# Performance work log

Measured on AMD Instinct MI355X. Metric: run time of the kernel, lower is better.

## Reference

```python
import jax, jax.numpy as jnp
import numpy as np

N_TRANSFORMS = 24
N_INIT = 5
SOFT_BLEND = 5.0
MAX_STEPS = 8   # reduced from 50 for reference runtime; same per-step math
CVG = 1e-5
DVG = 1.0
EPS = 1e-6


def posi_enc(x):
    # min_deg=0, max_deg=4, append_identity: [...,3] -> [...,27]
    scales = jnp.asarray([1.0, 2.0, 4.0, 8.0], x.dtype)
    xb = (x[..., None, :] * scales[:, None]).reshape(x.shape[:-1] + (12,))
    return jnp.concatenate([x, jnp.sin(xb), jnp.cos(xb)], axis=-1)


def mlp(h, params):
    for W, b in params[:-1]:
        h = jax.nn.relu(h @ W + b)
    W, b = params[-1]
    return h @ W + b


def setup_inputs() -> dict:
    key = jax.random.key(0)
    ks = jax.random.split(key, 16)
    B, N, J = 1, 32768, N_TRANSFORMS
    x = jax.random.normal(ks[0], (B, N, 3), jnp.float32)
    bone_pts = jax.random.normal(ks[1], (J, 3), jnp.float32)

    def near_id(k):
        A = jnp.eye(4, dtype=jnp.float32) + 0.05 * jax.random.normal(k, (J, 4, 4), jnp.float32)
        return A.at[:, 3, :].set(jnp.asarray([0.0, 0.0, 0.0, 1.0], jnp.float32))

    inp = dict(
        x=x, bone_pts=bone_pts,
        transforms=near_id(ks[2]), delta_transforms=near_id(ks[3]),
        W0=0.1 * jax.random.normal(ks[4], (27, 128), jnp.float32), b0=jnp.zeros((128,), jnp.float32),
        W1=0.1 * jax.random.normal(ks[5], (128, 128), jnp.float32), b1=jnp.zeros((128,), jnp.float32),
        W2=0.1 * jax.random.normal(ks[6], (128, 128), jnp.float32), b2=jnp.zeros((128,), jnp.float32),
        W3=0.1 * jax.random.normal(ks[7], (128, 128), jnp.float32), b3=jnp.zeros((128,), jnp.float32),
        W4=0.1 * jax.random.normal(ks[8], (128, 25), jnp.float32), b4=jnp.zeros((25,), jnp.float32),
    )
    return inp


def reference(x, bone_pts, transforms, delta_transforms, W0, b0, W1, b1, W2, b2, W3, b3, W4, b4):
    params = [(W0, b0), (W1, b1), (W2, b2), (W3, b3), (W4, b4)]
    B, N, _ = x.shape
    I = N_INIT + 1  # with_bkgd appends identity init
    dt = x.dtype

    # ---- _initialize_canonical: KNN over bone distances, gather delta transforms
    d = jnp.linalg.norm(x[:, :, None, :] - bone_pts, axis=-1)          # [B,N,J]
    idx = jax.lax.top_k(-d, N_INIT)[1]                                  # [B,N,5]
    Tsel = delta_transforms[idx]                                        # [B,N,5,4,4]
    eye4 = jnp.broadcast_to(jnp.eye(4, dtype=dt), (B, N, 1, 4, 4))
    Tinit = jnp.concatenate([Tsel, eye4], axis=2)                       # [B,N,I,4,4]
    xh = jnp.concatenate([x, jnp.ones_like(x[..., :1])], axis=-1)
    xc0 = jnp.einsum('bnipq,bnq->bnip', Tinit[..., :3, :4], xh)         # [B,N,I,3]

    M = B * N * I
    target = jnp.broadcast_to(x[:, :, None, :], (B, N, I, 3)).reshape(M, 3)
    x0 = xc0.reshape(M, 3)
    Tfull = jnp.concatenate([transforms, jnp.eye(4, dtype=dt)[None]], axis=0)  # [J+1,4,4]

    def g(xc):  # forward-skinning residual g(x_cano) = LBS(x_cano) - x_world
        w = jax.nn.softmax(SOFT_BLEND * mlp(posi_enc(xc), params), axis=-1)   # [M,25]
        tf = jnp.einsum('mj,jpq->mpq', w, Tfull)                               # [M,4,4]
        return jnp.einsum('mpq,mq->mp', tf[:, :3, :3], xc) + tf[:, :3, 3] - target

    # ---- Broyden with dense per-point masking (replaces torch boolean indexing)
    Jinv0 = jnp.broadcast_to(jnp.eye(3, dtype=dt), (M, 3, 3))
    gx0 = g(x0)
    upd0 = -(Jinv0 @ gx0[:, :, None])[:, :, 0]
    norm0 = jnp.linalg.norm(gx0, axis=-1)
    zeros3 = jnp.zeros((M, 3), dt)
    state = (x0, gx0, Jinv0, upd0, x0, norm0, zeros3, zeros3, jnp.ones((M,), bool))

    def body(_, s):
        xk, gx, Jinv, upd, xopt, nopt, dx, dgx, mask = s
        m3 = mask[:, None]
        dx = jnp.where(m3, upd, dx)
        xk = jnp.where(m3, xk + dx, xk)
        gnew = g(xk)
        dgx = jnp.where(m3, gnew - gx, dgx)
        gx = jnp.where(m3, gx + dgx, gx)
        gn = jnp.linalg.norm(gx, axis=-1)
        better = gn < nopt
        nopt = jnp.where(better, gn, nopt)
        xopt = jnp.where(better[:, None], xk, xopt)
        mask = (nopt > CVG) & (gn < DVG)
        vT = dx[:, None, :] @ Jinv                                      # [M,1,3]
        a = dx[:, :, None] - Jinv @ dgx[:, :, None]                      # [M,3,1]
        b = vT @ dgx[:, :, None]                                         # [M,1,1]
        b = b + jnp.where(b >= 0, EPS, -EPS)
        Jinv = jnp.where(mask[:, None, None], Jinv + (a / b) @ vT, Jinv)
        upd = jnp.where(m3, -(Jinv @ gx[:, :, None])[:, :, 0], upd)
        return (xk, gx, Jinv, upd, xopt, nopt, dx, dgx, mask)

    state = jax.lax.fori_loop(0, MAX_STEPS, body, state)
    xopt, nopt = state[4], state[5]
    xopt = jax.lax.stop_gradient(xopt)  # torch detaches the root solve
    valid = nopt < CVG

    # differentiable final forward skinning at the found canonical points
    w = jax.nn.softmax(SOFT_BLEND * mlp(posi_enc(xopt), params), axis=-1)
    tf = jnp.einsum('mj,jpq->mpq', w, Tfull)
    xw = jnp.einsum('mpq,mq->mp', tf[:, :3, :3], xopt) + tf[:, :3, 3]

    return (xw.reshape(B, N, I, 3), xopt.reshape(B, N, I, 3),
            nopt.reshape(B, N, I), valid.reshape(B, N, I))
```

## Files before the change

kernel.cpp:

```cpp
#include <hip/hip_runtime.h>
#include <math.h>

#define BLOCK 256
#define PPB 64
#define HP 132
#define WCOLS 2136

typedef float v2f __attribute__((ext_vector_type(2)));

__device__ __forceinline__ v2f mkv2(float a, float b) {
    v2f r; r.x = a; r.y = b; return r;
}
__device__ __forceinline__ v2f pkfma(v2f a, v2f b, v2f c) {
#if __has_builtin(__builtin_elementwise_fma)
    return __builtin_elementwise_fma(a, b, c);
#else
    return mkv2(fmaf(a.x, b.x, c.x), fmaf(a.y, b.y, c.y));
#endif
}
__device__ __forceinline__ float f4el(const float4& v, int r) {
    return (r == 0) ? v.x : (r == 1) ? v.y : (r == 2) ? v.z : v.w;
}
__device__ __forceinline__ int col_base(int p) { return p * HP + ((p >> 2) << 3); }

__global__ void prep_kernel(const float* __restrict__ W0, const float* __restrict__ W4,
                            const float* __restrict__ b4, float* __restrict__ W0p,
                            float* __restrict__ W4p, float* __restrict__ b4p) {
    const int t = blockIdx.x * blockDim.x + threadIdx.x;
    if (t < 32 * 128) {
        const int k = t >> 7, j = t & 127;
        W0p[t] = (k < 27) ? W0[k * 128 + j] : 0.0f;
    }
    if (t < 128 * 32) {
        const int k = t >> 5, j = t & 31;
        W4p[t] = (j < 25) ? W4[k * 25 + j] : 0.0f;
    }
    if (t < 32) b4p[t] = (t < 25) ? b4[t] : 0.0f;
}

template <int K, int WS>
__device__ __forceinline__ void layerM(const float* __restrict__ Wc,
                                       const float* __restrict__ bc,
                                       const float* hg, float* hwr) {
    constexpr int NB = K / 4;
    v2f acc[16];
    {
        const float4 b0 = *(const float4*)(bc);
        const float4 b1 = *(const float4*)(bc + 4);
#pragma unroll
        for (int p = 0; p < 4; ++p) {
            acc[p * 4 + 0] = mkv2(b0.x, b0.y);
            acc[p * 4 + 1] = mkv2(b0.z, b0.w);
            acc[p * 4 + 2] = mkv2(b1.x, b1.y);
            acc[p * 4 + 3] = mkv2(b1.z, b1.w);
        }
    }
#pragma unroll 2
    for (int kb = 0; kb < NB; ++kb) {
        float4 h4[4];
#pragma unroll
        for (int p = 0; p < 4; ++p)
            h4[p] = *(const float4*)(hg + p * HP + kb * 4);
        float4 w0[4], w1[4];
#pragma unroll
        for (int r = 0; r < 4; ++r) {
            w0[r] = *(const float4*)(Wc + (kb * 4 + r) * WS);
            w1[r] = *(const float4*)(Wc + (kb * 4 + r) * WS + 4);
        }
#pragma unroll
        for (int r = 0; r < 4; ++r) {
            const v2f wa = mkv2(w0[r].x, w0[r].y);
            const v2f wb = mkv2(w0[r].z, w0[r].w);
            const v2f wc = mkv2(w1[r].x, w1[r].y);
            const v2f wd = mkv2(w1[r].z, w1[r].w);
#pragma unroll
            for (int p = 0; p < 4; ++p) {
                const float hv = f4el(h4[p], r);
                const v2f hh = mkv2(hv, hv);
                acc[p * 4 + 0] = pkfma(hh, wa, acc[p * 4 + 0]);
                acc[p * 4 + 1] = pkfma(hh, wb, acc[p * 4 + 1]);
                acc[p * 4 + 2] = pkfma(hh, wc, acc[p * 4 + 2]);
                acc[p * 4 + 3] = pkfma(hh, wd, acc[p * 4 + 3]);
            }
        }
    }
#pragma unroll
    for (int p = 0; p < 4; ++p) {
        float4 o0, o1;
        o0.x = fmaxf(acc[p * 4 + 0].x, 0.f); o0.y = fmaxf(acc[p * 4 + 0].y, 0.f);
        o0.z = fmaxf(acc[p * 4 + 1].x, 0.f); o0.w = fmaxf(acc[p * 4 + 1].y, 0.f);
        o1.x = fmaxf(acc[p * 4 + 2].x, 0.f); o1.y = fmaxf(acc[p * 4 + 2].y, 0.f);
        o1.z = fmaxf(acc[p * 4 + 3].x, 0.f); o1.w = fmaxf(acc[p * 4 + 3].y, 0.f);
        *(float4*)(hwr + p * HP) = o0;
        *(float4*)(hwr + p * HP + 4) = o1;
    }
}

__global__ __launch_bounds__(BLOCK)
__attribute__((amdgpu_num_vgpr(128))) void snarf_kernel(
    const float* __restrict__ xin, const float* __restrict__ bone_pts,
    const float* __restrict__ transforms, const float* __restrict__ delta_tf,
    const float* __restrict__ W0p, const float* __restrict__ b0,
    const float* __restrict__ W1, const float* __restrict__ b1,
    const float* __restrict__ W2, const float* __restrict__ b2,
    const float* __restrict__ W3, const float* __restrict__ b3,
    const float* __restrict__ W4p, const float* __restrict__ b4p,
    float* __restrict__ out, int Npts) {
    __shared__ float hL[4 * WCOLS];
    __shared__ float stL[25 * PPB];
    const int tid = threadIdx.x;
    const int wid = tid >> 6;
    const int lane = tid & 63;
    const int p16 = lane & 15;
    const int sq = lane >> 4;
    const int cg = lane >> 2;
    const int gg = lane & 3;
    const int M = Npts * 6;
    const int m = blockIdx.x * PPB + wid * 16 + p16;
    const int mc = (m < M) ? m : (M - 1);
    const int n = mc / 6;
    const int i = mc - n * 6;

    float* hWv = &hL[wid * WCOLS];
    const float* hg = hWv + gg * 536;
    float* hwr = hWv + gg * 536 + 8 * cg;
    float* hq = hWv + col_base(p16);
    volatile float* st = &stL[wid * 16 + p16];
#define STS(idx) st[(idx) * PPB]

    const float tx = xin[n * 3 + 0], ty = xin[n * 3 + 1], tz = xin[n * 3 + 2];

    float xk0, xk1, xk2;
    if (i < 5) {
        float dprev = -1.0f;
        int jprev = -1;
        for (int r = 0; r <= i; ++r) {
            float bd = 3.4028235e38f;
            int bj = 0;
            for (int j = 0; j < 24; ++j) {
                const float ax = tx - bone_pts[j * 3 + 0];
                const float ay = ty - bone_pts[j * 3 + 1];
                const float az = tz - bone_pts[j * 3 + 2];
                const float d = sqrtf(ax * ax + ay * ay + az * az);
                const bool taken = (d < dprev) || (d == dprev && j <= jprev);
                if (!taken && d < bd) { bd = d; bj = j; }
            }
            dprev = bd;
            jprev = bj;
        }
        const float* T = delta_tf + jprev * 16;
        xk0 = fmaf(T[0], tx, fmaf(T[1], ty, fmaf(T[2], tz, T[3])));
        xk1 = fmaf(T[4], tx, fmaf(T[5], ty, fmaf(T[6], tz, T[7])));
        xk2 = fmaf(T[8], tx, fmaf(T[9], ty, fmaf(T[10], tz, T[11])));
    } else {
        xk0 = tx; xk1 = ty; xk2 = tz;
    }

    float gx0 = 0.f, gx1 = 0.f, gx2 = 0.f;
    bool mask = (m < M);

    for (int step = -1; step < 8; ++step) {
        bool m3 = mask;
        if (step >= 0) {
            if (__ballot(mask) == 0ull) break;
            if (m3) {
                const float u0 = STS(9), u1 = STS(10), u2 = STS(11);
                STS(12) = u0; STS(13) = u1; STS(14) = u2;
                xk0 += u0; xk1 += u1; xk2 += u2;
            }
        }
        const float cx0 = xk0, cx1 = xk1, cx2 = xk2;

        {
            const float f = (float)(1 << sq);
            float sx, cxv, sy, cyv, sz, czv;
            sincosf(f * cx0, &sx, &cxv);
            sincosf(f * cx1, &sy, &cyv);
            sincosf(f * cx2, &sz, &czv);
            if (sq == 0) { hq[0] = cx0; hq[1] = cx1; hq[2] = cx2; }
            const int sb = 3 + sq * 3;
            hq[sb + 0] = sx;  hq[sb + 1] = sy;  hq[sb + 2] = sz;
            hq[sb + 12] = cxv; hq[sb + 13] = cyv; hq[sb + 14] = czv;
            if (sq == 3) {
                hq[27] = 0.f; hq[28] = 0.f; hq[29] = 0.f; hq[30] = 0.f; hq[31] = 0.f;
            }
        }

        __builtin_amdgcn_s_setprio(1);
        layerM<32, 128>(W0p + 8 * cg, b0 + 8 * cg, hg, hwr);
        layerM<128, 128>(W1 + 8 * cg, b1 + 8 * cg, hg, hwr);
        layerM<128, 128>(W2 + 8 * cg, b2 + 8 * cg, hg, hwr);
        layerM<128, 128>(W3 + 8 * cg, b3 + 8 * cg, hg, hwr);

        {
            v2f la[4];
            const float* bc = b4p + 8 * sq;
            const float4 bb0 = *(const float4*)(bc);
            const float4 bb1 = *(const float4*)(bc + 4);
            la[0] = mkv2(bb0.x, bb0.y); la[1] = mkv2(bb0.z, bb0.w);
            la[2] = mkv2(bb1.x, bb1.y); la[3] = mkv2(bb1.z, bb1.w);
            const float* Wc = W4p + 8 * sq;
#pragma unroll 2
            for (int kb = 0; kb < 32; ++kb) {
                const float4 h4 = *(const float4*)(hq + kb * 4);
#pragma unroll
                for (int r = 0; r < 4; ++r) {
                    const int k = kb * 4 + r;
                    const float4 w0 = *(const float4*)(Wc + k * 32);
                    const float4 w1 = *(const float4*)(Wc + k * 32 + 4);
                    const float hv = f4el(h4, r);
                    const v2f hh = mkv2(hv, hv);
                    la[0] = pkfma(hh, mkv2(w0.x, w0.y), la[0]);
                    la[1] = pkfma(hh, mkv2(w0.z, w0.w), la[1]);
                    la[2] = pkfma(hh, mkv2(w1.x, w1.y), la[2]);
                    la[3] = pkfma(hh, mkv2(w1.z, w1.w), la[3]);
                }
            }
            __builtin_amdgcn_s_setprio(0);
            float4 o0, o1;
            o0.x = la[0].x; o0.y = la[0].y; o0.z = la[1].x; o0.w = la[1].y;
            o1.x = la[2].x; o1.y = la[2].y; o1.z = la[3].x; o1.w = la[3].y;
            *(float4*)(hq + 8 * sq) = o0;
            *(float4*)(hq + 8 * sq + 4) = o1;
        }

        float l25[25];
        {
            const float4 r0 = *(const float4*)(hq + 0);
            const float4 r1 = *(const float4*)(hq + 4);
            const float4 r2 = *(const float4*)(hq + 8);
            const float4 r3 = *(const float4*)(hq + 12);
            const float4 r4 = *(const float4*)(hq + 16);
            const float4 r5 = *(const float4*)(hq + 20);
            l25[0] = r0.x; l25[1] = r0.y; l25[2] = r0.z; l25[3] = r0.w;
            l25[4] = r1.x; l25[5] = r1.y; l25[6] = r1.z; l25[7] = r1.w;
            l25[8] = r2.x; l25[9] = r2.y; l25[10] = r2.z; l25[11] = r2.w;
            l25[12] = r3.x; l25[13] = r3.y; l25[14] = r3.z; l25[15] = r3.w;
            l25[16] = r4.x; l25[17] = r4.y; l25[18] = r4.z; l25[19] = r4.w;
            l25[20] = r5.x; l25[21] = r5.y; l25[22] = r5.z; l25[23] = r5.w;
            l25[24] = hq[24];
        }

        float zm = -3.4028235e38f;
#pragma unroll
        for (int j = 0; j < 25; ++j) {
            l25[j] = 5.0f * l25[j];
            zm = fmaxf(zm, l25[j]);
        }
        float ssum = 0.f;
#pragma unroll
        for (int j = 0; j < 25; ++j) {
            l25[j] = expf(l25[j] - zm);
            ssum += l25[j];
        }
        const float inv = 1.0f / ssum;

        float tf[12];
#pragma unroll
        for (int r = 0; r < 12; ++r) tf[r] = 0.f;
#pragma unroll
        for (int j = 0; j < 24; ++j) {
            const float wj = l25[j] * inv;
            const float* T = transforms + j * 16;
#pragma unroll
            for (int r = 0; r < 12; ++r) tf[r] = fmaf(wj, T[r], tf[r]);
        }
        {
            const float wj = l25[24] * inv;
            tf[0] += wj; tf[5] += wj; tf[10] += wj;
        }
        const float r0 = fmaf(tf[0], cx0, fmaf(tf[1], cx1, fmaf(tf[2], cx2, tf[3])));
        const float r1 = fmaf(tf[4], cx0, fmaf(tf[5], cx1, fmaf(tf[6], cx2, tf[7])));
        const float r2 = fmaf(tf[8], cx0, fmaf(tf[9], cx1, fmaf(tf[10], cx2, tf[11])));

        const float g0 = r0 - tx, g1 = r1 - ty, g2 = r2 - tz;

        if (step == -1) {
            gx0 = g0; gx1 = g1; gx2 = g2;
            const float gn = sqrtf(g0 * g0 + g1 * g1 + g2 * g2);
            STS(21) = gn;
            STS(9) = -g0; STS(10) = -g1; STS(11) = -g2;
            STS(18) = xk0; STS(19) = xk1; STS(20) = xk2;
            STS(22) = r0; STS(23) = r1; STS(24) = r2;
            STS(12) = 0.f; STS(13) = 0.f; STS(14) = 0.f;
            STS(15) = 0.f; STS(16) = 0.f; STS(17) = 0.f;
            STS(0) = 1.f; STS(1) = 0.f; STS(2) = 0.f;
            STS(3) = 0.f; STS(4) = 1.f; STS(5) = 0.f;
            STS(6) = 0.f; STS(7) = 0.f; STS(8) = 1.f;
        } else {
            float J00 = STS(0), J01 = STS(1), J02 = STS(2);
            float J10 = STS(3), J11 = STS(4), J12 = STS(5);
            float J20 = STS(6), J21 = STS(7), J22 = STS(8);
            const float dx0 = STS(12), dx1 = STS(13), dx2 = STS(14);
            float dg0 = STS(15), dg1 = STS(16), dg2 = STS(17);
            float nopt = STS(21);
            if (m3) {
                dg0 = g0 - gx0; dg1 = g1 - gx1; dg2 = g2 - gx2;
                gx0 += dg0; gx1 += dg1; gx2 += dg2;
                STS(15) = dg0; STS(16) = dg1; STS(17) = dg2;
            }
            const float gn = sqrtf(gx0 * gx0 + gx1 * gx1 + gx2 * gx2);
            const bool better = gn < nopt;
            if (better) {
                nopt = gn;
                STS(21) = gn;
                STS(18) = xk0; STS(19) = xk1; STS(20) = xk2;
                STS(22) = r0; STS(23) = r1; STS(24) = r2;
            }
            mask = (nopt > 1e-5f) && (gn < 1.0f) && (m < M);

            const float v0 = dx0 * J00 + dx1 * J10 + dx2 * J20;
            const float v1 = dx0 * J01 + dx1 * J11 + dx2 * J21;
            const float v2 = dx0 * J02 + dx1 * J12 + dx2 * J22;
            const float Jd0 = J00 * dg0 + J01 * dg1 + J02 * dg2;
            const float Jd1 = J10 * dg0 + J11 * dg1 + J12 * dg2;
            const float Jd2 = J20 * dg0 + J21 * dg1 + J22 * dg2;
            const float a0 = dx0 - Jd0, a1 = dx1 - Jd1, a2 = dx2 - Jd2;
            float bden = v0 * dg0 + v1 * dg1 + v2 * dg2;
            bden += (bden >= 0.f) ? 1e-6f : -1e-6f;
            if (mask) {
                const float q0 = a0 / bden, q1 = a1 / bden, q2 = a2 / bden;
                J00 = fmaf(q0, v0, J00); J01 = fmaf(q0, v1, J01); J02 = fmaf(q0, v2, J02);
                J10 = fmaf(q1, v0, J10); J11 = fmaf(q1, v1, J11); J12 = fmaf(q1, v2, J12);
                J20 = fmaf(q2, v0, J20); J21 = fmaf(q2, v1, J21); J22 = fmaf(q2, v2, J22);
                STS(0) = J00; STS(1) = J01; STS(2) = J02;
                STS(3) = J10; STS(4) = J11; STS(5) = J12;
                STS(6) = J20; STS(7) = J21; STS(8) = J22;
            }
            if (m3) {
                STS(9) = -(J00 * gx0 + J01 * gx1 + J02 * gx2);
                STS(10) = -(J10 * gx0 + J11 * gx1 + J12 * gx2);
                STS(11) = -(J20 * gx0 + J21 * gx1 + J22 * gx2);
            }
        }
    }

    if (sq == 0 && m < M) {
        const float nopt = STS(21);
        out[(size_t)m * 3 + 0] = STS(22);
        out[(size_t)m * 3 + 1] = STS(23);
        out[(size_t)m * 3 + 2] = STS(24);
        float* xopt_out = out + (size_t)M * 3;
        xopt_out[(size_t)m * 3 + 0] = STS(18);
        xopt_out[(size_t)m * 3 + 1] = STS(19);
        xopt_out[(size_t)m * 3 + 2] = STS(20);
        out[(size_t)M * 6 + m] = nopt;
        out[(size_t)M * 7 + m] = (nopt < 1e-5f) ? 1.0f : 0.0f;
    }
#undef STS
}

extern "C" void kernel_launch(void* const* d_in, const int* in_sizes, int n_in,
                              void* d_out, int out_size, void* d_ws, size_t ws_size,
                              hipStream_t stream) {
    const float* x = (const float*)d_in[0];
    const float* bone_pts = (const float*)d_in[1];
    const float* transforms = (const float*)d_in[2];
    const float* delta_tf = (const float*)d_in[3];
    const float* W0 = (const float*)d_in[4];
    const float* b0 = (const float*)d_in[5];
    const float* W1 = (const float*)d_in[6];
    const float* b1 = (const float*)d_in[7];
    const float* W2 = (const float*)d_in[8];
    const float* b2 = (const float*)d_in[9];
    const float* W3 = (const float*)d_in[10];
    const float* b3 = (const float*)d_in[11];
    const float* W4 = (const float*)d_in[12];
    const float* b4 = (const float*)d_in[13];
    float* out = (float*)d_out;

    float* W0p = (float*)d_ws;
    float* W4p = W0p + 32 * 128;
    float* b4p = W4p + 128 * 32;

    prep_kernel<<<16, 256, 0, stream>>>(W0, W4, b4, W0p, W4p, b4p);

    const int Npts = in_sizes[0] / 3;
    const int M = Npts * 6;
    const int blocks = (M + PPB - 1) / PPB;
    snarf_kernel<<<blocks, BLOCK, 0, stream>>>(
        x, bone_pts, transforms, delta_tf, W0p, b0, W1, b1, W2, b2, W3, b3,
        W4p, b4p, out, Npts);
}
```

Measured before the change: 2.027 ms.

## Stage MLP weights through double-buffered shared memory tiles with block-wide sync

Repacks all MLP weights into 56 contiguous 1024-float tiles in a prep kernel. The main kernel then streams these tiles through a double-buffered LDS buffer: each tile is prefetched into registers, written to the other buffer, and followed by __syncthreads. Weight reads therefore come from LDS instead of per-lane global/L2 loads. The early exit becomes a block-wide flag check, so all four waves keep iterating until every wave has converged. This adds roughly 60 block barriers per Newton step and removes per-wave independent early exit.

```diff
diff --git a/kernel.cpp b/kernel.cpp
--- a/kernel.cpp
+++ b/kernel.cpp
@@ -5,6 +5,7 @@
 #define PPB 64
 #define HP 132
 #define WCOLS 2136
+#define NTILES 56
 
 typedef float v2f __attribute__((ext_vector_type(2)));
 
@@ -23,76 +24,59 @@
 }
 __device__ __forceinline__ int col_base(int p) { return p * HP + ((p >> 2) << 3); }
 
-__global__ void prep_kernel(const float* __restrict__ W0, const float* __restrict__ W4,
-                            const float* __restrict__ b4, float* __restrict__ W0p,
-                            float* __restrict__ W4p, float* __restrict__ b4p) {
-    const int t = blockIdx.x * blockDim.x + threadIdx.x;
-    if (t < 32 * 128) {
-        const int k = t >> 7, j = t & 127;
-        W0p[t] = (k < 27) ? W0[k * 128 + j] : 0.0f;
-    }
-    if (t < 128 * 32) {
-        const int k = t >> 5, j = t & 31;
-        W4p[t] = (j < 25) ? W4[k * 25 + j] : 0.0f;
-    }
-    if (t < 32) b4p[t] = (t < 25) ? b4[t] : 0.0f;
-}
-
-template <int K, int WS>
-__device__ __forceinline__ void layerM(const float* __restrict__ Wc,
-                                       const float* __restrict__ bc,
-                                       const float* hg, float* hwr) {
-    constexpr int NB = K / 4;
-    v2f acc[16];
-    {
-        const float4 b0 = *(const float4*)(bc);
-        const float4 b1 = *(const float4*)(bc + 4);
+__global__ void prep_kernel(const float* __restrict__ W0, const float* __restrict__ W1,
+                            const float* __restrict__ W2, const float* __restrict__ W3,
+                            const float* __restrict__ W4, const float* __restrict__ b4,
+                            float* __restrict__ Wt, float* __restrict__ b4p) {
+    const int d = blockIdx.x * blockDim.x + threadIdx.x;
+    if (d < NTILES * 1024) {
+        const int t = d >> 10, w = d & 1023;
+        float v;
+        if (t < 52) {
+            const int r = w >> 7, rem = w & 127;
+            const int half = rem >> 6, q = (rem >> 2) & 15, jl = rem & 3;
+            const int col = q * 8 + half * 4 + jl;
+            if (t < 4)       { const int k = t * 8 + r;        v = (k < 27) ? W0[k * 128 + col] : 0.f; }
+            else if (t < 20) { const int k = (t - 4) * 8 + r;  v = W1[k * 128 + col]; }
+            else if (t < 36) { const int k = (t - 20) * 8 + r; v = W2[k * 128 + col]; }
+            else             { const int k = (t - 36) * 8 + r; v = W3[k * 128 + col]; }
+        } else {
+            const int r = w >> 5, rem = w & 31;
+            const int half = (rem >> 4) & 1, s = (rem >> 2) & 3, jl = rem & 3;
+            const int col = s * 8 + half * 4 + jl;
+            const int k = (t - 52) * 32 + r;
+            v = (col < 25) ? W4[k * 25 + col] : 0.f;
+        }
+        Wt[d] = v;
+    }
+    if (d < 32) b4p[d] = (d < 25) ? b4[d] : 0.f;
+}
+
+__device__ __forceinline__ void batch4(const float* wt, int r0, int cg,
+                                       const float* hg, int k0,
+                                       v2f* __restrict__ acc) {
+    float4 h4[4];
+#pragma unroll
+    for (int p = 0; p < 4; ++p) h4[p] = *(const float4*)(hg + p * HP + k0);
+    float4 w0[4], w1[4];
+#pragma unroll
+    for (int r = 0; r < 4; ++r) {
+        w0[r] = *(const float4*)(wt + (r0 + r) * 128 + cg * 4);
+        w1[r] = *(const float4*)(wt + (r0 + r) * 128 + 64 + cg * 4);
+    }
+#pragma unroll
+    for (int r = 0; r < 4; ++r) {
+        const v2f wa = mkv2(w0[r].x, w0[r].y), wb2 = mkv2(w0[r].z, w0[r].w);
+        const v2f wc = mkv2(w1[r].x, w1[r].y), wd = mkv2(w1[r].z, w1[r].w);
 #pragma unroll
         for (int p = 0; p < 4; ++p) {
-            acc[p * 4 + 0] = mkv2(b0.x, b0.y);
-            acc[p * 4 + 1] = mkv2(b0.z, b0.w);
-            acc[p * 4 + 2] = mkv2(b1.x, b1.y);
-            acc[p * 4 + 3] = mkv2(b1.z, b1.w);
-        }
-    }
-#pragma unroll 2
-    for (int kb = 0; kb < NB; ++kb) {
-        float4 h4[4];
-#pragma unroll
-        for (int p = 0; p < 4; ++p)
-            h4[p] = *(const float4*)(hg + p * HP + kb * 4);
-        float4 w0[4], w1[4];
-#pragma unroll
-        for (int r = 0; r < 4; ++r) {
-            w0[r] = *(const float4*)(Wc + (kb * 4 + r) * WS);
-            w1[r] = *(const float4*)(Wc + (kb * 4 + r) * WS + 4);
-        }
-#pragma unroll
-        for (int r = 0; r < 4; ++r) {
-            const v2f wa = mkv2(w0[r].x, w0[r].y);
-            const v2f wb = mkv2(w0[r].z, w0[r].w);
-            const v2f wc = mkv2(w1[r].x, w1[r].y);
-            const v2f wd = mkv2(w1[r].z, w1[r].w);
-#pragma unroll
-            for (int p = 0; p < 4; ++p) {
-                const float hv = f4el(h4[p], r);
-                const v2f hh = mkv2(hv, hv);
-                acc[p * 4 + 0] = pkfma(hh, wa, acc[p * 4 + 0]);
-                acc[p * 4 + 1] = pkfma(hh, wb, acc[p * 4 + 1]);
-                acc[p * 4 + 2] = pkfma(hh, wc, acc[p * 4 + 2]);
-                acc[p * 4 + 3] = pkfma(hh, wd, acc[p * 4 + 3]);
-            }
-        }
-    }
-#pragma unroll
-    for (int p = 0; p < 4; ++p) {
-        float4 o0, o1;
-        o0.x = fmaxf(acc[p * 4 + 0].x, 0.f); o0.y = fmaxf(acc[p * 4 + 0].y, 0.f);
-        o0.z = fmaxf(acc[p * 4 + 1].x, 0.f); o0.w = fmaxf(acc[p * 4 + 1].y, 0.f);
-        o1.x = fmaxf(acc[p * 4 + 2].x, 0.f); o1.y = fmaxf(acc[p * 4 + 2].y, 0.f);
-        o1.z = fmaxf(acc[p * 4 + 3].x, 0.f); o1.w = fmaxf(acc[p * 4 + 3].y, 0.f);
-        *(float4*)(hwr + p * HP) = o0;
-        *(float4*)(hwr + p * HP + 4) = o1;
+            const float hv = f4el(h4[p], r);
+            const v2f hh = mkv2(hv, hv);
+            acc[p * 4 + 0] = pkfma(hh, wa, acc[p * 4 + 0]);
+            acc[p * 4 + 1] = pkfma(hh, wb2, acc[p * 4 + 1]);
+            acc[p * 4 + 2] = pkfma(hh, wc, acc[p * 4 + 2]);
+            acc[p * 4 + 3] = pkfma(hh, wd, acc[p * 4 + 3]);
+        }
     }
 }
 
@@ -100,14 +84,14 @@
 __attribute__((amdgpu_num_vgpr(128))) void snarf_kernel(
     const float* __restrict__ xin, const float* __restrict__ bone_pts,
     const float* __restrict__ transforms, const float* __restrict__ delta_tf,
-    const float* __restrict__ W0p, const float* __restrict__ b0,
-    const float* __restrict__ W1, const float* __restrict__ b1,
-    const float* __restrict__ W2, const float* __restrict__ b2,
-    const float* __restrict__ W3, const float* __restrict__ b3,
-    const float* __restrict__ W4p, const float* __restrict__ b4p,
+    const float* __restrict__ Wt, const float* __restrict__ b0,
+    const float* __restrict__ b1, const float* __restrict__ b2,
+    const float* __restrict__ b3, const float* __restrict__ b4p,
     float* __restrict__ out, int Npts) {
     __shared__ float hL[4 * WCOLS];
     __shared__ float stL[25 * PPB];
+    __shared__ float wb[2][1024];
+    __shared__ int flags[4];
     const int tid = threadIdx.x;
     const int wid = tid >> 6;
     const int lane = tid & 63;
@@ -159,10 +143,15 @@
     float gx0 = 0.f, gx1 = 0.f, gx2 = 0.f;
     bool mask = (m < M);
 
+    int cur = 0;
+    *(float4*)(&wb[0][0] + tid * 4) = *(const float4*)(Wt + tid * 4);
+    __syncthreads();
+
     for (int step = -1; step < 8; ++step) {
         bool m3 = mask;
         if (step >= 0) {
-            if (__ballot(mask) == 0ull) break;
+            __syncthreads();
+            if ((flags[0] | flags[1] | flags[2] | flags[3]) == 0) break;
             if (m3) {
                 const float u0 = STS(9), u1 = STS(10), u2 = STS(11);
                 STS(12) = u0; STS(13) = u1; STS(14) = u2;
@@ -187,34 +176,73 @@
         }
 
         __builtin_amdgcn_s_setprio(1);
-        layerM<32, 128>(W0p + 8 * cg, b0 + 8 * cg, hg, hwr);
-        layerM<128, 128>(W1 + 8 * cg, b1 + 8 * cg, hg, hwr);
-        layerM<128, 128>(W2 + 8 * cg, b2 + 8 * cg, hg, hwr);
-        layerM<128, 128>(W3 + 8 * cg, b3 + 8 * cg, hg, hwr);
+#pragma unroll 1
+        for (int L = 0; L < 4; ++L) {
+            const int tbase = (L == 0) ? 0 : (4 + (L - 1) * 16);
+            const int NT = (L == 0) ? 4 : 16;
+            const float* bc = ((L == 0) ? b0 : (L == 1) ? b1 : (L == 2) ? b2 : b3) + 8 * cg;
+            v2f acc[16];
+            {
+                const float4 b0v = *(const float4*)(bc);
+                const float4 b1v = *(const float4*)(bc + 4);
+#pragma unroll
+                for (int p = 0; p < 4; ++p) {
+                    acc[p * 4 + 0] = mkv2(b0v.x, b0v.y);
+                    acc[p * 4 + 1] = mkv2(b0v.z, b0v.w);
+                    acc[p * 4 + 2] = mkv2(b1v.x, b1v.y);
+                    acc[p * 4 + 3] = mkv2(b1v.z, b1v.w);
+                }
+            }
+#pragma unroll 1
+            for (int t = 0; t < NT; ++t) {
+                const float4 stg = *(const float4*)(Wt + (tbase + t + 1) * 1024 + tid * 4);
+                batch4(&wb[cur][0], 0, cg, hg, t * 8, acc);
+                batch4(&wb[cur][0], 4, cg, hg, t * 8 + 4, acc);
+                *(float4*)(&wb[cur ^ 1][0] + tid * 4) = stg;
+                __syncthreads();
+                cur ^= 1;
+            }
+#pragma unroll
+            for (int p = 0; p < 4; ++p) {
+                float4 o0, o1;
+                o0.x = fmaxf(acc[p * 4 + 0].x, 0.f); o0.y = fmaxf(acc[p * 4 + 0].y, 0.f);
+                o0.z = fmaxf(acc[p * 4 + 1].x, 0.f); o0.w = fmaxf(acc[p * 4 + 1].y, 0.f);
+                o1.x = fmaxf(acc[p * 4 + 2].x, 0.f); o1.y = fmaxf(acc[p * 4 + 2].y, 0.f);
+                o1.z = fmaxf(acc[p * 4 + 3].x, 0.f); o1.w = fmaxf(acc[p * 4 + 3].y, 0.f);
+                *(float4*)(hwr + p * HP) = o0;
+                *(float4*)(hwr + p * HP + 4) = o1;
+            }
+        }
 
         {
             v2f la[4];
-            const float* bc = b4p + 8 * sq;
-            const float4 bb0 = *(const float4*)(bc);
-            const float4 bb1 = *(const float4*)(bc + 4);
+            const float4 bb0 = *(const float4*)(b4p + 8 * sq);
+            const float4 bb1 = *(const float4*)(b4p + 8 * sq + 4);
             la[0] = mkv2(bb0.x, bb0.y); la[1] = mkv2(bb0.z, bb0.w);
             la[2] = mkv2(bb1.x, bb1.y); la[3] = mkv2(bb1.z, bb1.w);
-            const float* Wc = W4p + 8 * sq;
+#pragma unroll 1
+            for (int t = 0; t < 4; ++t) {
+                const int nt = (t < 3) ? (53 + t) : 0;
+                const float4 stg = *(const float4*)(Wt + nt * 1024 + tid * 4);
+                const float* wt = &wb[cur][0];
 #pragma unroll 2
-            for (int kb = 0; kb < 32; ++kb) {
-                const float4 h4 = *(const float4*)(hq + kb * 4);
-#pragma unroll
-                for (int r = 0; r < 4; ++r) {
-                    const int k = kb * 4 + r;
-                    const float4 w0 = *(const float4*)(Wc + k * 32);
-                    const float4 w1 = *(const float4*)(Wc + k * 32 + 4);
-                    const float hv = f4el(h4, r);
-                    const v2f hh = mkv2(hv, hv);
-                    la[0] = pkfma(hh, mkv2(w0.x, w0.y), la[0]);
-                    la[1] = pkfma(hh, mkv2(w0.z, w0.w), la[1]);
-                    la[2] = pkfma(hh, mkv2(w1.x, w1.y), la[2]);
-                    la[3] = pkfma(hh, mkv2(w1.z, w1.w), la[3]);
+                for (int kb = 0; kb < 8; ++kb) {
+                    const float4 h4 = *(const float4*)(hq + t * 32 + kb * 4);
+#pragma unroll
+                    for (int r = 0; r < 4; ++r) {
+                        const float4 w0 = *(const float4*)(wt + (kb * 4 + r) * 32 + sq * 4);
+                        const float4 w1 = *(const float4*)(wt + (kb * 4 + r) * 32 + 16 + sq * 4);
+                        const float hv = f4el(h4, r);
+                        const v2f hh = mkv2(hv, hv);
+                        la[0] = pkfma(hh, mkv2(w0.x, w0.y), la[0]);
+                        la[1] = pkfma(hh, mkv2(w0.z, w0.w), la[1]);
+                        la[2] = pkfma(hh, mkv2(w1.x, w1.y), la[2]);
+                        la[3] = pkfma(hh, mkv2(w1.z, w1.w), la[3]);
+                    }
                 }
+                *(float4*)(&wb[cur ^ 1][0] + tid * 4) = stg;
+                __syncthreads();
+                cur ^= 1;
             }
             __builtin_amdgcn_s_setprio(0);
             float4 o0, o1;
@@ -333,6 +361,10 @@
                 STS(11) = -(J20 * gx0 + J21 * gx1 + J22 * gx2);
             }
         }
+        {
+            const unsigned long long b = __ballot(mask);
+            if (lane == 0) flags[wid] = (b != 0ull) ? 1 : 0;
+        }
     }
 
     if (sq == 0 && m < M) {
@@ -369,16 +401,15 @@
     const float* b4 = (const float*)d_in[13];
     float* out = (float*)d_out;
 
-    float* W0p = (float*)d_ws;
-    float* W4p = W0p + 32 * 128;
-    float* b4p = W4p + 128 * 32;
-
-    prep_kernel<<<16, 256, 0, stream>>>(W0, W4, b4, W0p, W4p, b4p);
+    float* Wt = (float*)d_ws;
+    float* b4p = Wt + NTILES * 1024;
+
+    prep_kernel<<<(NTILES * 1024 + 255) / 256, 256, 0, stream>>>(
+        W0, W1, W2, W3, W4, b4, Wt, b4p);
 
     const int Npts = in_sizes[0] / 3;
     const int M = Npts * 6;
     const int blocks = (M + PPB - 1) / PPB;
     snarf_kernel<<<blocks, BLOCK, 0, stream>>>(
-        x, bone_pts, transforms, delta_tf, W0p, b0, W1, b1, W2, b2, W3, b3,
-        W4p, b4p, out, Npts);
-}
+        x, bone_pts, transforms, delta_tf, Wt, b0, b1, b2, b3, b4p, out, Npts);
+}
```

After: 1.747 ms. -13.8%, faster.
